# Kernel optimization log

Measured on AMD Instinct MI355X. Metric: run time of the kernel, lower is better.

Reference implementation:

```python
import jax, jax.numpy as jnp
import numpy as np

B, N, F_IN, ENC = 512, 512, 6, 128
EPS = 1e-5  # BatchNorm1d default eps


def _masked_bn_relu(h, m, gamma, beta):
    # h: [B,N,C]; m: [B,N,1] float mask. BN stats over valid points only,
    # matching torch's first_mlp(x[mask]) gather semantics (biased variance).
    cnt = jnp.maximum(m.sum(), 1.0)
    mean = (h * m).sum(axis=(0, 1)) / cnt
    var = (jnp.square(h - mean) * m).sum(axis=(0, 1)) / cnt
    hn = (h - mean) * jax.lax.rsqrt(var + EPS) * gamma + beta
    return jax.nn.relu(hn)


def setup_inputs() -> dict:
    key = jax.random.key(0)
    ks = jax.random.split(key, 16)
    s = lambda fan_in: 1.0 / np.sqrt(fan_in)
    inp = {
        "x": jax.random.normal(ks[0], (B, N, F_IN), dtype=jnp.float32),
        "mask": jax.random.bernoulli(ks[1], 0.7, (B, N)),
        # first_mlp: Linear(F_IN,128), BN(128), ReLU, Linear(128,256)
        "W1": jax.random.uniform(ks[2], (F_IN, 128), jnp.float32, -s(F_IN), s(F_IN)),
        "b1": jnp.zeros((128,), jnp.float32),
        "g1": jnp.ones((128,), jnp.float32),
        "be1": jnp.zeros((128,), jnp.float32),
        "W2": jax.random.uniform(ks[3], (128, 256), jnp.float32, -s(128), s(128)),
        "b2": jnp.zeros((256,), jnp.float32),
        # second_mlp: Linear(512,256), BN(256), ReLU, Linear(256,ENC)
        "W3": jax.random.uniform(ks[4], (512, 256), jnp.float32, -s(512), s(512)),
        "b3": jnp.zeros((256,), jnp.float32),
        "g2": jnp.ones((256,), jnp.float32),
        "be2": jnp.zeros((256,), jnp.float32),
        "W4": jax.random.uniform(ks[5], (256, ENC), jnp.float32, -s(256), s(256)),
        "b4": jnp.zeros((ENC,), jnp.float32),
    }
    return inp


def reference(x, mask, W1, b1, g1, be1, W2, b2, W3, b3, g2, be2, W4, b4):
    m = mask[..., None].astype(x.dtype)  # [B,N,1]
    # first_mlp on valid points; invalid positions become zeros (scatter into zeros buffer)
    h = x @ W1 + b1
    h = _masked_bn_relu(h, m, g1, be1)
    h = (h @ W2 + b2) * m  # [B,N,256], zeros where mask is False
    pooled = h.max(axis=1)  # [B,256] (zeros participate, as in torch)
    feat = jnp.concatenate(
        [h, jnp.broadcast_to(pooled[:, None, :], (h.shape[0], h.shape[1], pooled.shape[-1]))],
        axis=-1,
    )  # [B,N,512]
    h2 = feat @ W3 + b3
    h2 = _masked_bn_relu(h2, m, g2, be2)
    h2 = (h2 @ W4 + b4) * m  # [B,N,ENC], zeros where invalid
    return h2.max(axis=1)  # [B,ENC]
```

## Files before the change

kernel.cpp:

```cpp
#include <hip/hip_runtime.h>
#include <stdint.h>

#define BB   512
#define NN   512
#define MROWS (BB*NN)
#define RT   (MROWS/64)
#define EPSV 1e-5f

typedef unsigned short u16;
typedef __attribute__((ext_vector_type(8))) short bf16x8;
typedef __attribute__((ext_vector_type(4))) float f32x4;

__device__ __forceinline__ float read_mask(const void* mp, int r, int mode) {
  if (mode == 0) return ((const unsigned char*)mp)[r] ? 1.f : 0.f;
  if (mode == 1) return ((const unsigned int*)mp)[r] ? 1.f : 0.f;
  return ((const unsigned long long*)mp)[r] ? 1.f : 0.f;
}

__device__ __forceinline__ u16 f2bf(float f) {
  union { float f; unsigned int u; } v; v.f = f;
  unsigned int u = v.u;
  return (u16)((u + 0x7FFFu + ((u >> 16) & 1u)) >> 16);
}

__device__ __forceinline__ float bf2f(u16 b) {
  union { unsigned int u; float f; } t;
  t.u = ((unsigned int)b) << 16;
  return t.f;
}

__device__ __forceinline__ unsigned int cvt_pk_bf16(float lo, float hi) {
  unsigned int r;
  asm("v_cvt_pk_bf16_f32 %0, %1, %2" : "=v"(r) : "v"(lo), "v"(hi));
  return r;
}

__global__ __launch_bounds__(256) void k_prep(
    const float* __restrict__ W2, const float* __restrict__ W3, const float* __restrict__ W4,
    const float* __restrict__ b2, const unsigned char* __restrict__ mu,
    u16* __restrict__ w2t, u16* __restrict__ w4t,
    u16* __restrict__ w23t, float* __restrict__ c23, int* __restrict__ mode) {
  __shared__ float row[256];
  __shared__ int c1s, c4s;
  const int blk = blockIdx.x;
  if (blk < 256) {
    const int idx = blk*256 + threadIdx.x;
    if (idx < 32768) {
      const int n = idx >> 7, k = idx & 127;
      w2t[idx] = f2bf(W2[(size_t)k*256 + n]);
    } else {
      const int j = idx - 32768;
      const int n = j >> 8, k = j & 255;
      w4t[j] = f2bf(W4[(size_t)k*128 + n]);
    }
  } else if (blk < 385) {
    const int n = threadIdx.x;
    const int k = blk - 256;
    if (k < 128) {
      row[n] = W2[(size_t)k*256 + n];
      __syncthreads();
      float a0 = 0.f, a1 = 0.f, a2v = 0.f, a3 = 0.f;
      for (int j = 0; j < 256; j += 4) {
        a0 = fmaf(row[j  ], W3[(size_t)(j    )*256 + n], a0);
        a1 = fmaf(row[j+1], W3[(size_t)(j + 1)*256 + n], a1);
        a2v= fmaf(row[j+2], W3[(size_t)(j + 2)*256 + n], a2v);
        a3 = fmaf(row[j+3], W3[(size_t)(j + 3)*256 + n], a3);
      }
      w23t[(size_t)n*128 + k] = f2bf(((a0 + a1) + (a2v + a3)));
    } else {
      float a0 = 0.f, a1 = 0.f, a2v = 0.f, a3 = 0.f;
      for (int j = 0; j < 256; j += 4) {
        a0 = fmaf(b2[j  ], W3[(size_t)(j    )*256 + n], a0);
        a1 = fmaf(b2[j+1], W3[(size_t)(j + 1)*256 + n], a1);
        a2v= fmaf(b2[j+2], W3[(size_t)(j + 2)*256 + n], a2v);
        a3 = fmaf(b2[j+3], W3[(size_t)(j + 3)*256 + n], a3);
      }
      c23[n] = ((a0 + a1) + (a2v + a3));
    }
  } else {
    if (threadIdx.x == 0) { c1s = 0; c4s = 0; }
    __syncthreads();
    for (int i = threadIdx.x; i < 4096; i += 256) {
      const unsigned char b = mu[i];
      if (b) {
        if ((i & 3) == 1) atomicAdd(&c1s, 1);
        if ((i & 7) == 4) atomicAdd(&c4s, 1);
      }
    }
    __syncthreads();
    if (threadIdx.x == 0) *mode = c1s ? 0 : (c4s ? 1 : 2);
  }
}

__global__ __launch_bounds__(256) void k_stats1(
    const float* __restrict__ x, const void* __restrict__ mask,
    const int* __restrict__ modep,
    float* __restrict__ part, float* __restrict__ cntbf) {
  const int mode = *modep;
  const int tid = threadIdx.x;
  const int blk = blockIdx.x;
  float sx[6] = {0,0,0,0,0,0};
  float sxx[21] = {0};
  float cntq[4] = {0,0,0,0};
#pragma unroll
  for (int it = 0; it < 8; ++it) {
    const int r = blk*2048 + it*256 + tid;
    const float mv = read_mask(mask, r, mode);
    const float* xr = x + (size_t)r*6;
    const float2 p0 = *(const float2*)(xr);
    const float2 p1 = *(const float2*)(xr + 2);
    const float2 p2 = *(const float2*)(xr + 4);
    float v[6] = {p0.x, p0.y, p1.x, p1.y, p2.x, p2.y};
    cntq[it >> 1] += mv;
    int idx = 0;
#pragma unroll
    for (int j = 0; j < 6; ++j) {
      sx[j] = fmaf(mv, v[j], sx[j]);
      const float mj = mv * v[j];
#pragma unroll
      for (int k = j; k < 6; ++k) { sxx[idx] = fmaf(mj, v[k], sxx[idx]); ++idx; }
    }
  }
  float vals[32];
#pragma unroll
  for (int j = 0; j < 6; ++j) vals[j] = sx[j];
#pragma unroll
  for (int j = 0; j < 21; ++j) vals[6 + j] = sxx[j];
  vals[27] = 0.f;
#pragma unroll
  for (int q = 0; q < 4; ++q) vals[28 + q] = cntq[q];
#pragma unroll
  for (int j = 0; j < 32; ++j) {
#pragma unroll
    for (int m = 1; m <= 32; m <<= 1)
      vals[j] += __shfl_xor(vals[j], m, 64);
  }
  __shared__ float red[4][32];
  const int wave = tid >> 6, lane = tid & 63;
  if (lane == 0) {
#pragma unroll
    for (int j = 0; j < 32; ++j) red[wave][j] = vals[j];
  }
  __syncthreads();
  if (tid < 32) {
    const float tot = red[0][tid] + red[1][tid] + red[2][tid] + red[3][tid];
    part[(size_t)blk*32 + tid] = tot;
    if (tid >= 28) cntbf[blk*4 + (tid - 28)] = tot;
  }
}

__global__ __launch_bounds__(128) void k_fin1(
    const float* __restrict__ part,
    const float* __restrict__ W1, const float* __restrict__ b1,
    const float* __restrict__ g1, const float* __restrict__ be1,
    u16* __restrict__ w1pb, float* __restrict__ c1p, float* __restrict__ cntf) {
  __shared__ float tot[32];
  const int t = threadIdx.x;
  if (t < 32) {
    float a0 = 0.f, a1 = 0.f, a2v = 0.f, a3 = 0.f;
    for (int i = 0; i < 128; i += 4) {
      a0 += part[(size_t)(i    )*32 + t];
      a1 += part[(size_t)(i + 1)*32 + t];
      a2v+= part[(size_t)(i + 2)*32 + t];
      a3 += part[(size_t)(i + 3)*32 + t];
    }
    tot[t] = (a0 + a1) + (a2v + a3);
  }
  __syncthreads();
  float cnt = tot[28] + tot[29] + tot[30] + tot[31];
  if (cnt < 1.f) cnt = 1.f;
  if (t == 0) *cntf = cnt;
  const int c = t;
  float w[6];
#pragma unroll
  for (int k = 0; k < 6; ++k) w[k] = W1[k*128 + c];
  float s1 = 0.f;
#pragma unroll
  for (int k = 0; k < 6; ++k) s1 = fmaf(w[k], tot[k], s1);
  s1 /= cnt;
  float q = 0.f;
  {
    int idx = 6;
#pragma unroll
    for (int j = 0; j < 6; ++j) {
      q = fmaf(w[j]*w[j], tot[idx], q); ++idx;
#pragma unroll
      for (int k = j + 1; k < 6; ++k) { q = fmaf(2.f*w[j]*w[k], tot[idx], q); ++idx; }
    }
  }
  float var = q / cnt - s1*s1; if (var < 0.f) var = 0.f;
  const float mean = b1[c] + s1;
  const float a = g1[c] * rsqrtf(var + EPSV);
  c1p[c] = fmaf(b1[c], a, be1[c] - mean*a);
  {
    uint4 z0;
    z0.x = cvt_pk_bf16(w[0]*a, w[1]*a);
    z0.y = cvt_pk_bf16(w[2]*a, w[3]*a);
    z0.z = cvt_pk_bf16(w[4]*a, w[5]*a);
    z0.w = 0u;
    uint4 zz = {0u, 0u, 0u, 0u};
    *(uint4*)(w1pb + (size_t)c*32     ) = z0;
    *(uint4*)(w1pb + (size_t)c*32 +  8) = zz;
    *(uint4*)(w1pb + (size_t)c*32 + 16) = zz;
    *(uint4*)(w1pb + (size_t)c*32 + 24) = zz;
  }
}

__global__ __launch_bounds__(256, 4) void k_mega(
    const float* __restrict__ x, const void* __restrict__ mask, const int* __restrict__ modep,
    const u16* __restrict__ w1pb, const float* __restrict__ c1p,
    const u16* __restrict__ W2t, const float* __restrict__ b2,
    const u16* __restrict__ W23t, const float* __restrict__ c23,
    u16* __restrict__ acc3buf, float* __restrict__ poolpart,
    float* __restrict__ s2sum, float* __restrict__ s2sq) {
  __shared__ u16 buf[64*264];
  __shared__ float mk[64];
  u16* xb = buf + 64*136;
  const int mode = *modep;
  const int tid = threadIdx.x;
  const int rt = blockIdx.x;
  const int row0 = rt*64;
  const int b = rt >> 3, seg = rt & 7;
  if (tid < 64) {
    const float* xr = x + (size_t)(row0 + tid)*6;
    const float2 p0 = *(const float2*)(xr);
    const float2 p1 = *(const float2*)(xr + 2);
    const float2 p2 = *(const float2*)(xr + 4);
    uint4 z0;
    z0.x = cvt_pk_bf16(p0.x, p0.y);
    z0.y = cvt_pk_bf16(p1.x, p1.y);
    z0.z = cvt_pk_bf16(p2.x, p2.y);
    z0.w = 0u;
    uint4 zz = {0u, 0u, 0u, 0u};
    *(uint4*)(xb + tid*40     ) = z0;
    *(uint4*)(xb + tid*40 +  8) = zz;
    *(uint4*)(xb + tid*40 + 16) = zz;
    *(uint4*)(xb + tid*40 + 24) = zz;
    mk[tid] = read_mask(mask, row0 + tid, mode);
  }
  __syncthreads();
  const int wave = tid >> 6, lane = tid & 63;
  const int lr = lane & 15, lq = lane >> 4;
  {
    bf16x8 afr[4];
#pragma unroll
    for (int r = 0; r < 4; ++r)
      afr[r] = *(const bf16x8*)(xb + (r*16 + lr)*40 + lq*8);
    f32x4 acc[4][2];
#pragma unroll
    for (int r = 0; r < 4; ++r)
#pragma unroll
      for (int c = 0; c < 2; ++c) acc[r][c] = (f32x4){0.f,0.f,0.f,0.f};
#pragma unroll
    for (int c = 0; c < 2; ++c) {
      const bf16x8 bfr = *(const bf16x8*)(w1pb + (size_t)(wave*32 + c*16 + lr)*32 + lq*8);
#pragma unroll
      for (int r = 0; r < 4; ++r)
        acc[r][c] = __builtin_amdgcn_mfma_f32_16x16x32_bf16(bfr, afr[r], acc[r][c], 0, 0, 0);
    }
#pragma unroll
    for (int c = 0; c < 2; ++c) {
      const int colb = wave*32 + c*16 + lq*4;
      const float4 cc = *(const float4*)(c1p + colb);
#pragma unroll
      for (int r = 0; r < 4; ++r) {
        const int row = r*16 + lr;
        uint2 z;
        z.x = cvt_pk_bf16(fmaxf(acc[r][c][0] + cc.x, 0.f), fmaxf(acc[r][c][1] + cc.y, 0.f));
        z.y = cvt_pk_bf16(fmaxf(acc[r][c][2] + cc.z, 0.f), fmaxf(acc[r][c][3] + cc.w, 0.f));
        *(uint2*)(buf + row*136 + colb) = z;
      }
    }
  }
  __syncthreads();
  {
    f32x4 acc[4][4];
#pragma unroll
    for (int r = 0; r < 4; ++r)
#pragma unroll
      for (int c = 0; c < 4; ++c) acc[r][c] = (f32x4){0.f,0.f,0.f,0.f};
#pragma unroll
    for (int kc = 0; kc < 128; kc += 32) {
      bf16x8 afr[4];
#pragma unroll
      for (int r = 0; r < 4; ++r)
        afr[r] = *(const bf16x8*)(buf + (r*16 + lr)*136 + kc + lq*8);
#pragma unroll
      for (int c = 0; c < 4; ++c) {
        const bf16x8 bfr = *(const bf16x8*)(W2t + (size_t)(wave*64 + c*16 + lr)*128 + kc + lq*8);
#pragma unroll
        for (int r = 0; r < 4; ++r)
          acc[r][c] = __builtin_amdgcn_mfma_f32_16x16x32_bf16(afr[r], bfr, acc[r][c], 0, 0, 0);
      }
    }
#pragma unroll
    for (int c = 0; c < 4; ++c) {
      const int col = wave*64 + c*16 + lr;
      const float bb = b2[col];
      float cm = -1e38f;
#pragma unroll
      for (int r = 0; r < 4; ++r) {
        const int base = r*16 + lq*4;
#pragma unroll
        for (int i = 0; i < 4; ++i)
          cm = fmaxf(cm, (acc[r][c][i] + bb) * mk[base + i]);
      }
      cm = fmaxf(cm, __shfl_xor(cm, 16, 64));
      cm = fmaxf(cm, __shfl_xor(cm, 32, 64));
      if (lq == 0) poolpart[((size_t)(b*8 + seg))*256 + col] = cm;
    }
  }
  f32x4 acc3[4][4];
#pragma unroll
  for (int r = 0; r < 4; ++r)
#pragma unroll
    for (int c = 0; c < 4; ++c) acc3[r][c] = (f32x4){0.f,0.f,0.f,0.f};
#pragma unroll
  for (int kc = 0; kc < 128; kc += 32) {
    bf16x8 afr[4];
#pragma unroll
    for (int r = 0; r < 4; ++r)
      afr[r] = *(const bf16x8*)(buf + (r*16 + lr)*136 + kc + lq*8);
#pragma unroll
    for (int c = 0; c < 4; ++c) {
      const bf16x8 bfr = *(const bf16x8*)(W23t + (size_t)(wave*64 + c*16 + lr)*128 + kc + lq*8);
#pragma unroll
      for (int r = 0; r < 4; ++r)
        acc3[r][c] = __builtin_amdgcn_mfma_f32_16x16x32_bf16(afr[r], bfr, acc3[r][c], 0, 0, 0);
    }
  }
  __syncthreads();
#pragma unroll
  for (int c = 0; c < 4; ++c) {
    const int col = wave*64 + c*16 + lr;
    const float cc3 = c23[col];
    float sS = 0.f, sQ = 0.f;
#pragma unroll
    for (int r = 0; r < 4; ++r) {
      const int base = r*16 + lq*4;
#pragma unroll
      for (int i = 0; i < 4; i += 2) {
        const float a0 = (acc3[r][c][i]   + cc3) * mk[base + i];
        const float a1 = (acc3[r][c][i+1] + cc3) * mk[base + i + 1];
        const unsigned int u = cvt_pk_bf16(a0, a1);
        buf[(base + i    )*264 + col] = (u16)u;
        buf[(base + i + 1)*264 + col] = (u16)(u >> 16);
        sS += a0 + a1;
        sQ += a0*a0 + a1*a1;
      }
    }
    sS += __shfl_xor(sS, 16, 64);
    sS += __shfl_xor(sS, 32, 64);
    sQ += __shfl_xor(sQ, 16, 64);
    sQ += __shfl_xor(sQ, 32, 64);
    if (lq == 0) {
      s2sum[(size_t)rt*256 + col] = sS;
      s2sq [(size_t)rt*256 + col] = sQ;
    }
  }
  __syncthreads();
  for (int it = tid; it < 64*32; it += 256) {
    const int row = it >> 5, c8 = it & 31;
    *(uint4*)(acc3buf + (size_t)(row0 + row)*256 + c8*8) = *(const uint4*)(buf + row*264 + c8*8);
  }
}

__global__ __launch_bounds__(512) void k_poolP(
    const float* __restrict__ poolpart, const float* __restrict__ W3,
    const float* __restrict__ b3, float* __restrict__ P) {
  __shared__ float pl[256];
  __shared__ float part2[256];
  const int b = blockIdx.x, tid = threadIdx.x;
  if (tid < 256) {
    float m = poolpart[((size_t)b*8)*256 + tid];
#pragma unroll
    for (int s = 1; s < 8; ++s) m = fmaxf(m, poolpart[((size_t)(b*8+s))*256 + tid]);
    pl[tid] = m;
  }
  __syncthreads();
  const int col = tid & 255, half = tid >> 8;
  const int cbase = half*128;
  float a0 = 0.f, a1 = 0.f, a2v = 0.f, a3 = 0.f;
  for (int c = cbase; c < cbase + 128; c += 4) {
    a0 = fmaf(pl[c  ], W3[(size_t)(256 + c    )*256 + col], a0);
    a1 = fmaf(pl[c+1], W3[(size_t)(256 + c + 1)*256 + col], a1);
    a2v= fmaf(pl[c+2], W3[(size_t)(256 + c + 2)*256 + col], a2v);
    a3 = fmaf(pl[c+3], W3[(size_t)(256 + c + 3)*256 + col], a3);
  }
  const float sum = (a0 + a1) + (a2v + a3);
  if (half == 1) part2[col] = sum;
  __syncthreads();
  if (half == 0) P[(size_t)b*256 + col] = sum + part2[col] + b3[col];
}

__global__ __launch_bounds__(256) void k_red2(
    const float* __restrict__ s2sum, const float* __restrict__ s2sq,
    const float* __restrict__ cntbf, const float* __restrict__ P,
    float* __restrict__ midS, float* __restrict__ midQ) {
  const int slab = blockIdx.x;
  const int c = threadIdx.x;
  float accS = 0.f, accQ = 0.f;
  for (int b = slab*8; b < slab*8 + 8; ++b) {
    const float cntb = cntbf[b];
    float S = 0.f, Q = 0.f;
#pragma unroll
    for (int s = 0; s < 8; ++s) {
      S += s2sum[(size_t)(b*8 + s)*256 + c];
      Q += s2sq [(size_t)(b*8 + s)*256 + c];
    }
    const float p = P[(size_t)b*256 + c];
    accS += fmaf(cntb, p, S);
    accQ += fmaf(cntb, p*p, fmaf(2.f*p, S, Q));
  }
  midS[slab*256 + c] = accS;
  midQ[slab*256 + c] = accQ;
}

__global__ __launch_bounds__(256) void k_fin2(
    const float* __restrict__ midS, const float* __restrict__ midQ,
    const float* __restrict__ cntf,
    const float* __restrict__ g2, const float* __restrict__ be2,
    float* __restrict__ a2, float* __restrict__ sh2) {
  const int c = threadIdx.x;
  float s = 0.f, q = 0.f;
#pragma unroll 8
  for (int k = 0; k < 64; ++k) { s += midS[k*256 + c]; q += midQ[k*256 + c]; }
  const float cf = *cntf;
  const float mean = s / cf;
  float var = q / cf - mean*mean; if (var < 0.f) var = 0.f;
  const float a = g2[c] * rsqrtf(var + EPSV);
  a2[c]  = a;
  sh2[c] = be2[c] - mean*a;
}

__global__ __launch_bounds__(512, 4) void k_gemm4(
    const u16* __restrict__ acc3buf, const void* __restrict__ mask, const int* __restrict__ modep,
    const float* __restrict__ P, const float* __restrict__ a2, const float* __restrict__ sh2,
    const u16* __restrict__ W4t, const float* __restrict__ b4,
    float* __restrict__ outpart) {
  __shared__ u16 a2t[64*264];
  __shared__ float a2l[256], s2b[256];
  __shared__ float mk[64];
  const int mode = *modep;
  const int tid = threadIdx.x;
  const int b = blockIdx.x >> 1;
  const int half = blockIdx.x & 1;
  const int wave = tid >> 6, lane = tid & 63;
  const int lr = lane & 15, lq = lane >> 4;
  const size_t rowbase = (size_t)b*512 + half*256;
  if (tid < 256) {
    const float aa = a2[tid];
    a2l[tid] = aa;
    s2b[tid] = fmaf(P[(size_t)b*256 + tid], aa, sh2[tid]);
  }
  bf16x8 bw[8];
#pragma unroll
  for (int j = 0; j < 8; ++j)
    bw[j] = *(const bf16x8*)(W4t + (size_t)(wave*16 + lr)*256 + j*32 + lq*8);
  const float bb = b4[wave*16 + lr];
  float cm = -1e38f;
  uint4 u[4];
#pragma unroll
  for (int it = 0; it < 4; ++it) {
    const int j = tid + it*512;
    u[it] = *(const uint4*)(acc3buf + (rowbase + (j >> 5))*256 + (j & 31)*8);
  }
  for (int seg = 0; seg < 4; ++seg) {
    __syncthreads();
#pragma unroll
    for (int it = 0; it < 4; ++it) {
      const int j = tid + it*512;
      const int row = j >> 5, c8 = j & 31;
      const u16* us = (const u16*)&u[it];
      unsigned int pk[4];
#pragma unroll
      for (int jj = 0; jj < 4; ++jj) {
        const int cc0 = c8*8 + jj*2, cc1 = cc0 + 1;
        const float z0 = fmaf(bf2f(us[jj*2    ]), a2l[cc0], s2b[cc0]);
        const float z1 = fmaf(bf2f(us[jj*2 + 1]), a2l[cc1], s2b[cc1]);
        pk[jj] = cvt_pk_bf16(fmaxf(z0, 0.f), fmaxf(z1, 0.f));
      }
      *(uint4*)(a2t + row*264 + c8*8) = *(const uint4*)pk;
    }
    if (tid < 64) mk[tid] = read_mask(mask, (int)(rowbase + seg*64 + tid), mode);
    if (seg < 3) {
#pragma unroll
      for (int it = 0; it < 4; ++it) {
        const int j = tid + it*512;
        u[it] = *(const uint4*)(acc3buf + (rowbase + (seg + 1)*64 + (j >> 5))*256 + (j & 31)*8);
      }
    }
    __syncthreads();
    f32x4 acc[4];
#pragma unroll
    for (int r = 0; r < 4; ++r) acc[r] = (f32x4){0.f,0.f,0.f,0.f};
#pragma unroll
    for (int kc8 = 0; kc8 < 8; ++kc8) {
      bf16x8 afr[4];
#pragma unroll
      for (int r = 0; r < 4; ++r)
        afr[r] = *(const bf16x8*)(a2t + (r*16 + lr)*264 + kc8*32 + lq*8);
#pragma unroll
      for (int r = 0; r < 4; ++r)
        acc[r] = __builtin_amdgcn_mfma_f32_16x16x32_bf16(afr[r], bw[kc8], acc[r], 0, 0, 0);
    }
#pragma unroll
    for (int r = 0; r < 4; ++r) {
#pragma unroll
      for (int i = 0; i < 4; ++i)
        cm = fmaxf(cm, (acc[r][i] + bb) * mk[r*16 + lq*4 + i]);
    }
  }
  cm = fmaxf(cm, __shfl_xor(cm, 16, 64));
  cm = fmaxf(cm, __shfl_xor(cm, 32, 64));
  if (lq == 0) outpart[(size_t)blockIdx.x*128 + wave*16 + lr] = cm;
}

__global__ __launch_bounds__(256) void k_outred2(
    const float* __restrict__ outpart, float* __restrict__ out) {
  const int idx = blockIdx.x*256 + threadIdx.x;
  const int b = idx >> 7, e = idx & 127;
  out[idx] = fmaxf(outpart[(size_t)(b*2)*128 + e], outpart[(size_t)(b*2 + 1)*128 + e]);
}

extern "C" void kernel_launch(void* const* d_in, const int* in_sizes, int n_in,
                              void* d_out, int out_size, void* d_ws, size_t ws_size,
                              hipStream_t stream) {
  const float* x    = (const float*)d_in[0];
  const void*  mask = d_in[1];
  const float* W1   = (const float*)d_in[2];
  const float* b1   = (const float*)d_in[3];
  const float* g1   = (const float*)d_in[4];
  const float* be1  = (const float*)d_in[5];
  const float* W2   = (const float*)d_in[6];
  const float* b2   = (const float*)d_in[7];
  const float* W3   = (const float*)d_in[8];
  const float* b3   = (const float*)d_in[9];
  const float* g2   = (const float*)d_in[10];
  const float* be2  = (const float*)d_in[11];
  const float* W4   = (const float*)d_in[12];
  const float* b4   = (const float*)d_in[13];
  float* out = (float*)d_out;

  char* ws = (char*)d_ws;
  size_t off = 0;
  auto take = [&](size_t bytes) -> char* {
    char* p = ws + off;
    off = (off + bytes + 255) & ~(size_t)255;
    return p;
  };
  u16*   acc3buf = (u16*)  take((size_t)MROWS*256*2);
  float* part    = (float*)take((size_t)128*32*4);
  float* cntbf   = (float*)take((size_t)512*4);
  u16*   w1pb    = (u16*)  take((size_t)128*32*2);
  float* c1p     = (float*)take(128*4);
  float* cntf    = (float*)take(256);
  float* poolpart= (float*)take((size_t)512*8*256*4);
  float* P       = (float*)take((size_t)512*256*4);
  float* s2sum   = (float*)take((size_t)RT*256*4);
  float* s2sq    = (float*)take((size_t)RT*256*4);
  float* midS    = (float*)take((size_t)64*256*4);
  float* midQ    = (float*)take((size_t)64*256*4);
  float* a2      = (float*)take(256*4);
  float* sh2     = (float*)take(256*4);
  float* outpart = (float*)take((size_t)1024*128*4);
  int*   modep   = (int*)  take(256);
  u16*   w2t     = (u16*)  take((size_t)256*128*2);
  u16*   w23t    = (u16*)  take((size_t)256*128*2);
  u16*   w4t     = (u16*)  take((size_t)128*256*2);
  float* c23     = (float*)take(256*4);

  k_prep<<<386, 256, 0, stream>>>(W2, W3, W4, b2, (const unsigned char*)mask,
                                  w2t, w4t, w23t, c23, modep);
  k_stats1<<<128, 256, 0, stream>>>(x, mask, modep, part, cntbf);
  k_fin1<<<1, 128, 0, stream>>>(part, W1, b1, g1, be1, w1pb, c1p, cntf);
  k_mega<<<RT, 256, 0, stream>>>(x, mask, modep, w1pb, c1p, w2t, b2, w23t, c23,
                                 acc3buf, poolpart, s2sum, s2sq);
  k_poolP<<<512, 512, 0, stream>>>(poolpart, W3, b3, P);
  k_red2<<<64, 256, 0, stream>>>(s2sum, s2sq, cntbf, P, midS, midQ);
  k_fin2<<<1, 256, 0, stream>>>(midS, midQ, cntf, g2, be2, a2, sh2);
  k_gemm4<<<1024, 512, 0, stream>>>(acc3buf, mask, modep, P, a2, sh2, w4t, b4, outpart);
  k_outred2<<<256, 256, 0, stream>>>(outpart, out);
}
```

Before: 238.8 us.

## Fold finalize kernels into last-block reductions and use atomic max output

Removes three small launches (k_fin1, k_fin2, k_outred2). The first two become a last-block-done step: an atomic counter picks the final block of k_stats1 and k_red2, which then runs the finalize math. The output reduction becomes a float atomic-max via CAS into an output that k_prep pre-fills with a large negative value. This trades launch gaps for atomics and threadfences, and it relies on k_prep resetting the counters on every call.

```diff
diff --git a/kernel.cpp b/kernel.cpp
--- a/kernel.cpp
+++ b/kernel.cpp
@@ -35,11 +35,24 @@
   return r;
 }
 
+__device__ __forceinline__ float aload(float* p) { return atomicAdd(p, 0.f); }
+
+__device__ __forceinline__ void atomicMaxF(float* addr, float val) {
+  unsigned int* ua = (unsigned int*)addr;
+  unsigned int old = __float_as_uint(*addr);
+  while (__uint_as_float(old) < val) {
+    unsigned int assumed = old;
+    old = atomicCAS(ua, assumed, __float_as_uint(val));
+    if (old == assumed) break;
+  }
+}
+
 __global__ __launch_bounds__(256) void k_prep(
     const float* __restrict__ W2, const float* __restrict__ W3, const float* __restrict__ W4,
     const float* __restrict__ b2, const unsigned char* __restrict__ mu,
     u16* __restrict__ w2t, u16* __restrict__ w4t,
-    u16* __restrict__ w23t, float* __restrict__ c23, int* __restrict__ mode) {
+    u16* __restrict__ w23t, float* __restrict__ c23, int* __restrict__ mode,
+    int* __restrict__ ctr1, int* __restrict__ ctr2, float* __restrict__ out) {
   __shared__ float row[256];
   __shared__ int c1s, c4s;
   const int blk = blockIdx.x;
@@ -77,8 +90,8 @@
       }
       c23[n] = ((a0 + a1) + (a2v + a3));
     }
-  } else {
-    if (threadIdx.x == 0) { c1s = 0; c4s = 0; }
+  } else if (blk == 385) {
+    if (threadIdx.x == 0) { c1s = 0; c4s = 0; *ctr1 = 0; *ctr2 = 0; }
     __syncthreads();
     for (int i = threadIdx.x; i < 4096; i += 256) {
       const unsigned char b = mu[i];
@@ -89,13 +102,23 @@
     }
     __syncthreads();
     if (threadIdx.x == 0) *mode = c1s ? 0 : (c4s ? 1 : 2);
+  } else {
+    const int idx = (blk - 386)*256 + threadIdx.x;
+    out[idx] = -1e38f;
   }
 }
 
 __global__ __launch_bounds__(256) void k_stats1(
     const float* __restrict__ x, const void* __restrict__ mask,
     const int* __restrict__ modep,
-    float* __restrict__ part, float* __restrict__ cntbf) {
+    float* __restrict__ part, float* __restrict__ cntbf,
+    const float* __restrict__ W1, const float* __restrict__ b1,
+    const float* __restrict__ g1, const float* __restrict__ be1,
+    u16* __restrict__ w1pb, float* __restrict__ c1p, float* __restrict__ cntf,
+    int* __restrict__ ctr1) {
+  __shared__ float red[4][32];
+  __shared__ float tot[32];
+  __shared__ int lastd;
   const int mode = *modep;
   const int tid = threadIdx.x;
   const int blk = blockIdx.x;
@@ -135,7 +158,6 @@
     for (int m = 1; m <= 32; m <<= 1)
       vals[j] += __shfl_xor(vals[j], m, 64);
   }
-  __shared__ float red[4][32];
   const int wave = tid >> 6, lane = tid & 63;
   if (lane == 0) {
 #pragma unroll
@@ -143,66 +165,58 @@
   }
   __syncthreads();
   if (tid < 32) {
-    const float tot = red[0][tid] + red[1][tid] + red[2][tid] + red[3][tid];
-    part[(size_t)blk*32 + tid] = tot;
-    if (tid >= 28) cntbf[blk*4 + (tid - 28)] = tot;
-  }
-}
-
-__global__ __launch_bounds__(128) void k_fin1(
-    const float* __restrict__ part,
-    const float* __restrict__ W1, const float* __restrict__ b1,
-    const float* __restrict__ g1, const float* __restrict__ be1,
-    u16* __restrict__ w1pb, float* __restrict__ c1p, float* __restrict__ cntf) {
-  __shared__ float tot[32];
-  const int t = threadIdx.x;
-  if (t < 32) {
-    float a0 = 0.f, a1 = 0.f, a2v = 0.f, a3 = 0.f;
-    for (int i = 0; i < 128; i += 4) {
-      a0 += part[(size_t)(i    )*32 + t];
-      a1 += part[(size_t)(i + 1)*32 + t];
-      a2v+= part[(size_t)(i + 2)*32 + t];
-      a3 += part[(size_t)(i + 3)*32 + t];
-    }
-    tot[t] = (a0 + a1) + (a2v + a3);
-  }
-  __syncthreads();
-  float cnt = tot[28] + tot[29] + tot[30] + tot[31];
-  if (cnt < 1.f) cnt = 1.f;
-  if (t == 0) *cntf = cnt;
-  const int c = t;
-  float w[6];
-#pragma unroll
-  for (int k = 0; k < 6; ++k) w[k] = W1[k*128 + c];
-  float s1 = 0.f;
-#pragma unroll
-  for (int k = 0; k < 6; ++k) s1 = fmaf(w[k], tot[k], s1);
-  s1 /= cnt;
-  float q = 0.f;
-  {
-    int idx = 6;
-#pragma unroll
-    for (int j = 0; j < 6; ++j) {
-      q = fmaf(w[j]*w[j], tot[idx], q); ++idx;
-#pragma unroll
-      for (int k = j + 1; k < 6; ++k) { q = fmaf(2.f*w[j]*w[k], tot[idx], q); ++idx; }
-    }
-  }
-  float var = q / cnt - s1*s1; if (var < 0.f) var = 0.f;
-  const float mean = b1[c] + s1;
-  const float a = g1[c] * rsqrtf(var + EPSV);
-  c1p[c] = fmaf(b1[c], a, be1[c] - mean*a);
-  {
-    uint4 z0;
-    z0.x = cvt_pk_bf16(w[0]*a, w[1]*a);
-    z0.y = cvt_pk_bf16(w[2]*a, w[3]*a);
-    z0.z = cvt_pk_bf16(w[4]*a, w[5]*a);
-    z0.w = 0u;
-    uint4 zz = {0u, 0u, 0u, 0u};
-    *(uint4*)(w1pb + (size_t)c*32     ) = z0;
-    *(uint4*)(w1pb + (size_t)c*32 +  8) = zz;
-    *(uint4*)(w1pb + (size_t)c*32 + 16) = zz;
-    *(uint4*)(w1pb + (size_t)c*32 + 24) = zz;
+    const float t2 = red[0][tid] + red[1][tid] + red[2][tid] + red[3][tid];
+    part[(size_t)blk*32 + tid] = t2;
+    if (tid >= 28) cntbf[blk*4 + (tid - 28)] = t2;
+  }
+  __threadfence();
+  __syncthreads();
+  if (tid == 0) lastd = atomicAdd(ctr1, 1);
+  __syncthreads();
+  if (lastd == 127) {
+    if (tid < 32) {
+      float s = 0.f;
+      for (int i = 0; i < 128; ++i) s += aload(&part[(size_t)i*32 + tid]);
+      tot[tid] = s;
+    }
+    __syncthreads();
+    if (tid < 128) {
+      float cnt = tot[28] + tot[29] + tot[30] + tot[31];
+      if (cnt < 1.f) cnt = 1.f;
+      if (tid == 0) *cntf = cnt;
+      const int c = tid;
+      float w[6];
+#pragma unroll
+      for (int k = 0; k < 6; ++k) w[k] = W1[k*128 + c];
+      float s1 = 0.f;
+#pragma unroll
+      for (int k = 0; k < 6; ++k) s1 = fmaf(w[k], tot[k], s1);
+      s1 /= cnt;
+      float q = 0.f;
+      {
+        int idx = 6;
+#pragma unroll
+        for (int j = 0; j < 6; ++j) {
+          q = fmaf(w[j]*w[j], tot[idx], q); ++idx;
+#pragma unroll
+          for (int k = j + 1; k < 6; ++k) { q = fmaf(2.f*w[j]*w[k], tot[idx], q); ++idx; }
+        }
+      }
+      float var = q / cnt - s1*s1; if (var < 0.f) var = 0.f;
+      const float mean = b1[c] + s1;
+      const float a = g1[c] * rsqrtf(var + EPSV);
+      c1p[c] = fmaf(b1[c], a, be1[c] - mean*a);
+      uint4 z0;
+      z0.x = cvt_pk_bf16(w[0]*a, w[1]*a);
+      z0.y = cvt_pk_bf16(w[2]*a, w[3]*a);
+      z0.z = cvt_pk_bf16(w[4]*a, w[5]*a);
+      z0.w = 0u;
+      uint4 zz = {0u, 0u, 0u, 0u};
+      *(uint4*)(w1pb + (size_t)c*32     ) = z0;
+      *(uint4*)(w1pb + (size_t)c*32 +  8) = zz;
+      *(uint4*)(w1pb + (size_t)c*32 + 16) = zz;
+      *(uint4*)(w1pb + (size_t)c*32 + 24) = zz;
+    }
   }
 }
 
@@ -396,7 +410,11 @@
 __global__ __launch_bounds__(256) void k_red2(
     const float* __restrict__ s2sum, const float* __restrict__ s2sq,
     const float* __restrict__ cntbf, const float* __restrict__ P,
-    float* __restrict__ midS, float* __restrict__ midQ) {
+    float* __restrict__ midS, float* __restrict__ midQ,
+    const float* __restrict__ cntf,
+    const float* __restrict__ g2, const float* __restrict__ be2,
+    float* __restrict__ a2, float* __restrict__ sh2, int* __restrict__ ctr2) {
+  __shared__ int lastd;
   const int slab = blockIdx.x;
   const int c = threadIdx.x;
   float accS = 0.f, accQ = 0.f;
@@ -412,32 +430,32 @@
     accS += fmaf(cntb, p, S);
     accQ += fmaf(cntb, p*p, fmaf(2.f*p, S, Q));
   }
-  midS[slab*256 + c] = accS;
-  midQ[slab*256 + c] = accQ;
-}
-
-__global__ __launch_bounds__(256) void k_fin2(
-    const float* __restrict__ midS, const float* __restrict__ midQ,
-    const float* __restrict__ cntf,
-    const float* __restrict__ g2, const float* __restrict__ be2,
-    float* __restrict__ a2, float* __restrict__ sh2) {
-  const int c = threadIdx.x;
-  float s = 0.f, q = 0.f;
-#pragma unroll 8
-  for (int k = 0; k < 64; ++k) { s += midS[k*256 + c]; q += midQ[k*256 + c]; }
-  const float cf = *cntf;
-  const float mean = s / cf;
-  float var = q / cf - mean*mean; if (var < 0.f) var = 0.f;
-  const float a = g2[c] * rsqrtf(var + EPSV);
-  a2[c]  = a;
-  sh2[c] = be2[c] - mean*a;
+  midS[(size_t)slab*256 + c] = accS;
+  midQ[(size_t)slab*256 + c] = accQ;
+  __threadfence();
+  __syncthreads();
+  if (c == 0) lastd = atomicAdd(ctr2, 1);
+  __syncthreads();
+  if (lastd == 63) {
+    float s = 0.f, q = 0.f;
+    for (int k = 0; k < 64; ++k) {
+      s += aload(&midS[(size_t)k*256 + c]);
+      q += aload(&midQ[(size_t)k*256 + c]);
+    }
+    const float cf = *cntf;
+    const float mean = s / cf;
+    float var = q / cf - mean*mean; if (var < 0.f) var = 0.f;
+    const float a = g2[c] * rsqrtf(var + EPSV);
+    a2[c]  = a;
+    sh2[c] = be2[c] - mean*a;
+  }
 }
 
 __global__ __launch_bounds__(512, 4) void k_gemm4(
     const u16* __restrict__ acc3buf, const void* __restrict__ mask, const int* __restrict__ modep,
     const float* __restrict__ P, const float* __restrict__ a2, const float* __restrict__ sh2,
     const u16* __restrict__ W4t, const float* __restrict__ b4,
-    float* __restrict__ outpart) {
+    float* __restrict__ out) {
   __shared__ u16 a2t[64*264];
   __shared__ float a2l[256], s2b[256];
   __shared__ float mk[64];
@@ -513,14 +531,7 @@
   }
   cm = fmaxf(cm, __shfl_xor(cm, 16, 64));
   cm = fmaxf(cm, __shfl_xor(cm, 32, 64));
-  if (lq == 0) outpart[(size_t)blockIdx.x*128 + wave*16 + lr] = cm;
-}
-
-__global__ __launch_bounds__(256) void k_outred2(
-    const float* __restrict__ outpart, float* __restrict__ out) {
-  const int idx = blockIdx.x*256 + threadIdx.x;
-  const int b = idx >> 7, e = idx & 127;
-  out[idx] = fmaxf(outpart[(size_t)(b*2)*128 + e], outpart[(size_t)(b*2 + 1)*128 + e]);
+  if (lq == 0) atomicMaxF(&out[(size_t)b*128 + wave*16 + lr], cm);
 }
 
 extern "C" void kernel_launch(void* const* d_in, const int* in_sizes, int n_in,
@@ -563,22 +574,22 @@
   float* midQ    = (float*)take((size_t)64*256*4);
   float* a2      = (float*)take(256*4);
   float* sh2     = (float*)take(256*4);
-  float* outpart = (float*)take((size_t)1024*128*4);
   int*   modep   = (int*)  take(256);
+  int*   ctr1    = (int*)  take(256);
+  int*   ctr2    = (int*)  take(256);
   u16*   w2t     = (u16*)  take((size_t)256*128*2);
   u16*   w23t    = (u16*)  take((size_t)256*128*2);
   u16*   w4t     = (u16*)  take((size_t)128*256*2);
   float* c23     = (float*)take(256*4);
 
-  k_prep<<<386, 256, 0, stream>>>(W2, W3, W4, b2, (const unsigned char*)mask,
-                                  w2t, w4t, w23t, c23, modep);
-  k_stats1<<<128, 256, 0, stream>>>(x, mask, modep, part, cntbf);
-  k_fin1<<<1, 128, 0, stream>>>(part, W1, b1, g1, be1, w1pb, c1p, cntf);
+  k_prep<<<642, 256, 0, stream>>>(W2, W3, W4, b2, (const unsigned char*)mask,
+                                  w2t, w4t, w23t, c23, modep, ctr1, ctr2, out);
+  k_stats1<<<128, 256, 0, stream>>>(x, mask, modep, part, cntbf,
+                                    W1, b1, g1, be1, w1pb, c1p, cntf, ctr1);
   k_mega<<<RT, 256, 0, stream>>>(x, mask, modep, w1pb, c1p, w2t, b2, w23t, c23,
                                  acc3buf, poolpart, s2sum, s2sq);
   k_poolP<<<512, 512, 0, stream>>>(poolpart, W3, b3, P);
-  k_red2<<<64, 256, 0, stream>>>(s2sum, s2sq, cntbf, P, midS, midQ);
-  k_fin2<<<1, 256, 0, stream>>>(midS, midQ, cntf, g2, be2, a2, sh2);
-  k_gemm4<<<1024, 512, 0, stream>>>(acc3buf, mask, modep, P, a2, sh2, w4t, b4, outpart);
-  k_outred2<<<256, 256, 0, stream>>>(outpart, out);
-}
+  k_red2<<<64, 256, 0, stream>>>(s2sum, s2sq, cntbf, P, midS, midQ,
+                                 cntf, g2, be2, a2, sh2, ctr2);
+  k_gemm4<<<1024, 512, 0, stream>>>(acc3buf, mask, modep, P, a2, sh2, w4t, b4, out);
+}
```

Result: slower. 253.4 us (+6.1%).
